# Performance work log

Measured on AMD Instinct MI355X. Metric: run time of the kernel, lower is better.

Reference implementation:

```python
import jax, jax.numpy as jnp
import numpy as np

DIM = 256
N_EMBED = 1024
COMMITMENT_COST = 0.25


def setup_inputs() -> dict:
    key = jax.random.key(0)
    k1, k2 = jax.random.split(key)
    z = jax.random.normal(k1, (16, 256, 64, 64), dtype=jnp.float32)
    # nn.Embedding weight initialized uniform(-1/n_embed, 1/n_embed)
    embed = jax.random.uniform(k2, (N_EMBED, DIM), dtype=jnp.float32,
                               minval=-1.0 / N_EMBED, maxval=1.0 / N_EMBED)
    return {"z": z, "embed": embed}


def reference(z, embed):
    sg = jax.lax.stop_gradient
    # NCHW -> NHWC, flatten spatial+batch to tokens
    zp = jnp.transpose(z, (0, 2, 3, 1))            # [B,H,W,C]
    zf = zp.reshape(-1, DIM)                        # [N, C]
    # squared euclidean distances via expansion: |z|^2 + |e|^2 - 2 z.e
    d = (jnp.sum(zf * zf, axis=1, keepdims=True)
         + jnp.sum(embed * embed, axis=1)
         - 2.0 * zf @ embed.T)                      # [N, K]
    idx = jnp.argmin(d, axis=1)                     # [N]
    min_encodings = jax.nn.one_hot(idx, N_EMBED, dtype=zf.dtype)  # [N, K]
    # direct gather == one-hot @ embed (same math, one HBM pass)
    z_q = embed[idx].reshape(zp.shape)              # [B,H,W,C]
    loss = (jnp.mean((sg(z_q) - zp) ** 2)
            + COMMITMENT_COST * jnp.mean((z_q - sg(zp)) ** 2))
    # straight-through estimator
    z_q_st = zp + sg(z_q - zp)
    e_mean = jnp.mean(min_encodings, axis=0)
    perplexity = jnp.exp(-jnp.sum(e_mean * jnp.log(e_mean + 1e-10)))
    z_q_out = jnp.transpose(z_q_st, (0, 3, 1, 2))   # back to NCHW
    return (loss, z_q_out, perplexity, min_encodings, idx[:, None])
```

## Files before the change

kernel.cpp:

```cpp
#include <hip/hip_runtime.h>
#include <math.h>

#define DIM    256
#define K_EMB  1024
#define HW     4096
#define CHW    1048576
#define N_TOK  65536
#define NELEM  16777216

#define OUT_LOSS 0
#define OUT_ZQ   1
#define OUT_PERP 16777217
#define OUT_MENC 16777218LL
#define OUT_IDX  83886082

#define TAU  1.5e-4f
#define WIN  6e-4f

typedef short short8  __attribute__((ext_vector_type(8)));
typedef float floatx4 __attribute__((ext_vector_type(4)));

#define A_OFF     2LL
#define EH_OFF    (A_OFF + 16777216LL)
#define FLAGS_OFF (EH_OFF + 131072LL)
#define SB_OFF    33554430LL

__device__ __forceinline__ unsigned short f2bf(float f) {
    unsigned int u = __float_as_uint(f);
    return (unsigned short)((u + 0x7FFFu + ((u >> 16) & 1u)) >> 16);
}
__device__ __forceinline__ float bf2f(unsigned short h) {
    return __uint_as_float(((unsigned int)h) << 16);
}

__device__ __forceinline__ float np_pair128(const float* p) {
    float r[8];
    #pragma unroll
    for (int j = 0; j < 8; ++j) r[j] = p[j];
    for (int i = 8; i < 128; i += 8)
        #pragma unroll
        for (int j = 0; j < 8; ++j) r[j] = __fadd_rn(r[j], p[i + j]);
    return __fadd_rn(__fadd_rn(__fadd_rn(r[0], r[1]), __fadd_rn(r[2], r[3])),
                     __fadd_rn(__fadd_rn(r[4], r[5]), __fadd_rn(r[6], r[7])));
}
__device__ __forceinline__ float np_pair256(const float* p) {
    return __fadd_rn(np_pair128(p), np_pair128(p + 128));
}

__global__ void t2_np_kernel(const float* __restrict__ embed, float* __restrict__ t2,
                             unsigned short* __restrict__ Eh) {
    int k = blockIdx.x * 256 + threadIdx.x;
    if (k >= K_EMB) return;
    const float* e = embed + (size_t)k * DIM;
    float p[256];
    for (int c = 0; c < DIM; c += 4) {
        float4 v = *(const float4*)(e + c);
        p[c]     = __fmul_rn(v.x, v.x);
        p[c + 1] = __fmul_rn(v.y, v.y);
        p[c + 2] = __fmul_rn(v.z, v.z);
        p[c + 3] = __fmul_rn(v.w, v.w);
    }
    t2[k] = np_pair256(p);
    unsigned short* dst = Eh + (size_t)k * DIM;
    for (int c0 = 0; c0 < DIM; c0 += 8) {
        short8 vh;
        #pragma unroll
        for (int u = 0; u < 8; ++u) vh[u] = (short)f2bf(e[c0 + u]);
        *(short8*)(dst + c0) = vh;
    }
}

__global__ void prep_z(const float* __restrict__ z, unsigned short* __restrict__ Ap) {
    const int tid = threadIdx.x;
    const int w   = tid & 63;
    const int j   = tid >> 6;
    const int n   = blockIdx.x * 64 + w;
    const int b   = n >> 12;
    const int rem = n & 4095;
    const float* zp = z + (size_t)b * CHW + rem;
    unsigned short* dst = Ap + (size_t)n * 512;
    for (int g = 0; g < 8; ++g) {
        int c0 = j * 64 + g * 8;
        short8 vh, vl;
        #pragma unroll
        for (int u = 0; u < 8; ++u) {
            float v = zp[(size_t)(c0 + u) * HW];
            unsigned short h = f2bf(v);
            vh[u] = (short)h;
            vl[u] = (short)f2bf(v - bf2f(h));
        }
        *(short8*)(dst + c0)       = vh;
        *(short8*)(dst + 256 + c0) = vl;
    }
}

__launch_bounds__(256, 4)
__global__ void vq_mfma(const unsigned short* __restrict__ Ap,
                        const unsigned short* __restrict__ Eh,
                        const float* __restrict__ t2g,
                        float* __restrict__ out,
                        unsigned int* __restrict__ nflag,
                        int* __restrict__ flags,
                        unsigned short* __restrict__ Sb) {
    __shared__ unsigned short lds_b[32 * 264];
    __shared__ float t2_lds[K_EMB];
    __shared__ unsigned short score_lds[64 * 40];

    const int tid  = threadIdx.x;
    const int lane = tid & 63;
    const int wv   = tid >> 6;
    const int l15  = lane & 15;
    const int quad = lane >> 4;
    const int m0   = blockIdx.x * 64;

    for (int i = tid; i < K_EMB; i += 256) t2_lds[i] = t2g[i];

    short8 a[16];
    const short8* arow = (const short8*)(Ap + (size_t)(m0 + wv * 16 + l15) * 512);
    #pragma unroll
    for (int kc = 0; kc < 16; ++kc) a[kc] = arow[kc * 4 + quad];

    float bs[4], ss[4]; int bk[4];
    float sc0[4], sc1[4];
    #pragma unroll
    for (int r = 0; r < 4; ++r) { bs[r] = 3.4e38f; ss[r] = 3.4e38f; bk[r] = 0; }

    const int srow = tid >> 3;
    const int scol = (tid & 7) * 32;
    const int tt = tid >> 2, ch = tid & 3;

    for (int it = 0; it < 32; ++it) {
        const int n0 = it * 32;
        __syncthreads();
        {
            const short8* g = (const short8*)(Eh + (size_t)(n0 + srow) * 256 + scol);
            short8* l = (short8*)(lds_b + srow * 264 + scol);
            short8 v0 = g[0], v1 = g[1], v2 = g[2], v3 = g[3];
            l[0] = v0; l[1] = v1; l[2] = v2; l[3] = v3;
        }
        if (it > 0) {
            #pragma unroll
            for (int r = 0; r < 4; ++r) {
                int row = wv * 16 + quad * 4 + r;
                score_lds[row * 40 + l15]      = f2bf(sc0[r]);
                score_lds[row * 40 + 16 + l15] = f2bf(sc1[r]);
            }
        }
        __syncthreads();
        if (it > 0) {
            short8 v = *(short8*)(score_lds + tt * 40 + ch * 8);
            *(short8*)(Sb + (size_t)(m0 + tt) * 1024 + (n0 - 32) + ch * 8) = v;
        }
        floatx4 acc0 = {0.f, 0.f, 0.f, 0.f};
        floatx4 acc1 = {0.f, 0.f, 0.f, 0.f};
        #pragma unroll
        for (int kc = 0; kc < 8; ++kc) {
            short8 b0 = *(const short8*)(lds_b + l15 * 264 + kc * 32 + quad * 8);
            short8 b1 = *(const short8*)(lds_b + (16 + l15) * 264 + kc * 32 + quad * 8);
            acc0 = __builtin_amdgcn_mfma_f32_16x16x32_bf16(a[kc],     b0, acc0, 0, 0, 0);
            acc1 = __builtin_amdgcn_mfma_f32_16x16x32_bf16(a[kc],     b1, acc1, 0, 0, 0);
            acc0 = __builtin_amdgcn_mfma_f32_16x16x32_bf16(a[8 + kc], b0, acc0, 0, 0, 0);
            acc1 = __builtin_amdgcn_mfma_f32_16x16x32_bf16(a[8 + kc], b1, acc1, 0, 0, 0);
        }
        float t20 = t2_lds[n0 + l15];
        float t21 = t2_lds[n0 + 16 + l15];
        #pragma unroll
        for (int r = 0; r < 4; ++r) {
            float s0 = fmaf(-2.0f, acc0[r], t20);
            sc0[r] = s0;
            if (s0 < bs[r]) { ss[r] = bs[r]; bs[r] = s0; bk[r] = n0 + l15; }
            else if (s0 < ss[r]) ss[r] = s0;
            float s1 = fmaf(-2.0f, acc1[r], t21);
            sc1[r] = s1;
            if (s1 < bs[r]) { ss[r] = bs[r]; bs[r] = s1; bk[r] = n0 + 16 + l15; }
            else if (s1 < ss[r]) ss[r] = s1;
        }
    }
    __syncthreads();
    #pragma unroll
    for (int r = 0; r < 4; ++r) {
        int row = wv * 16 + quad * 4 + r;
        score_lds[row * 40 + l15]      = f2bf(sc0[r]);
        score_lds[row * 40 + 16 + l15] = f2bf(sc1[r]);
    }
    __syncthreads();
    {
        short8 v = *(short8*)(score_lds + tt * 40 + ch * 8);
        *(short8*)(Sb + (size_t)(m0 + tt) * 1024 + 992 + ch * 8) = v;
    }

    #pragma unroll
    for (int r = 0; r < 4; ++r) {
        for (int mo = 1; mo < 16; mo <<= 1) {
            float obs = __shfl_xor(bs[r], mo, 64);
            float oss = __shfl_xor(ss[r], mo, 64);
            int   obk = __shfl_xor(bk[r], mo, 64);
            if (obs < bs[r] || (obs == bs[r] && obk < bk[r])) {
                ss[r] = fminf(bs[r], oss); bs[r] = obs; bk[r] = obk;
            } else {
                ss[r] = fminf(ss[r], obs);
            }
        }
        if (l15 == 0) {
            int ntok = m0 + wv * 16 + quad * 4 + r;
            out[OUT_IDX + ntok] = (float)bk[r];
            if (ss[r] - bs[r] < TAU) {
                unsigned int slot = atomicAdd(nflag, 1u);
                flags[slot] = ntok;
            }
        }
    }
}

__launch_bounds__(256)
__global__ void refine_v2(const float* __restrict__ z, const float* __restrict__ embed,
                          const float* __restrict__ t2g, float* __restrict__ out,
                          const unsigned int* __restrict__ nflag,
                          const int* __restrict__ flags,
                          const unsigned short* __restrict__ Sb) {
    __shared__ float pp4[4][256];
    __shared__ int   ccnt[4];
    __shared__ int   clist[4][32];

    const int lane = threadIdx.x & 63;
    const int wv   = threadIdx.x >> 6;
    const int wid  = blockIdx.x * 4 + wv;
    const int nf   = (int)*nflag;

    for (int i = wid; i < nf; i += gridDim.x * 4) {
        const int n   = flags[i];
        const int b   = n >> 12;
        const int rem = n & 4095;

        const unsigned short* srow = Sb + (size_t)n * 1024;
        short8 u0 = *(const short8*)(srow + lane * 16);
        short8 u1 = *(const short8*)(srow + lane * 16 + 8);
        float sv[16];
        #pragma unroll
        for (int j = 0; j < 8; ++j) { sv[j] = bf2f((unsigned short)u0[j]); sv[8 + j] = bf2f((unsigned short)u1[j]); }
        float lmin = sv[0];
        #pragma unroll
        for (int j = 1; j < 16; ++j) lmin = fminf(lmin, sv[j]);
        for (int mo = 1; mo < 64; mo <<= 1) lmin = fminf(lmin, __shfl_xor(lmin, mo, 64));
        const float thr = lmin + WIN;

        if (lane == 0) ccnt[wv] = 0;
        __asm__ volatile("s_waitcnt lgkmcnt(0)" ::: "memory");
        #pragma unroll
        for (int j = 0; j < 16; ++j) {
            if (sv[j] <= thr) {
                int pos = atomicAdd(&ccnt[wv], 1);
                if (pos < 32) clist[wv][pos] = lane * 16 + j;
            }
        }
        __asm__ volatile("s_waitcnt lgkmcnt(0)" ::: "memory");
        int cnt = ccnt[wv];
        if (cnt > 32) cnt = 32;

        const float* zt = z + (size_t)b * CHW + rem;
        double zd[4]; float zf[4];
        #pragma unroll
        for (int u = 0; u < 4; ++u) {
            float v = zt[(size_t)(lane + u * 64) * HW];
            zf[u] = v; zd[u] = (double)v;
            pp4[wv][lane + u * 64] = __fmul_rn(v, v);
        }
        __asm__ volatile("s_waitcnt lgkmcnt(0)" ::: "memory");
        float rj = 0.0f;
        if (lane < 16) {
            int jj = lane & 7, half = lane >> 3;
            const float* p = &pp4[wv][half * 128 + jj];
            rj = p[0];
            #pragma unroll
            for (int ii = 1; ii < 16; ++ii) rj = __fadd_rn(rj, p[ii * 8]);
        }
        float v0 = __shfl(rj, 0, 64), v1 = __shfl(rj, 1, 64), v2 = __shfl(rj, 2, 64), v3 = __shfl(rj, 3, 64);
        float v4 = __shfl(rj, 4, 64), v5 = __shfl(rj, 5, 64), v6 = __shfl(rj, 6, 64), v7 = __shfl(rj, 7, 64);
        float h0 = __fadd_rn(__fadd_rn(__fadd_rn(v0, v1), __fadd_rn(v2, v3)),
                             __fadd_rn(__fadd_rn(v4, v5), __fadd_rn(v6, v7)));
        v0 = __shfl(rj,  8, 64); v1 = __shfl(rj,  9, 64); v2 = __shfl(rj, 10, 64); v3 = __shfl(rj, 11, 64);
        v4 = __shfl(rj, 12, 64); v5 = __shfl(rj, 13, 64); v6 = __shfl(rj, 14, 64); v7 = __shfl(rj, 15, 64);
        float h1 = __fadd_rn(__fadd_rn(__fadd_rn(v0, v1), __fadd_rn(v2, v3)),
                             __fadd_rn(__fadd_rn(v4, v5), __fadd_rn(v6, v7)));
        const float t1 = __fadd_rn(h0, h1);

        float bd = 3.4e38f; int bkk = 1 << 30;
        for (int ci = 0; ci < cnt; ++ci) {
            int k = clist[wv][ci];
            const float* e = embed + (size_t)k * DIM;
            double s = 0.0;
            #pragma unroll
            for (int u = 0; u < 4; ++u) s = fma(zd[u], (double)e[lane + u * 64], s);
            for (int mo = 1; mo < 64; mo <<= 1) s += __shfl_xor(s, mo, 64);
            float rho = (float)s;
            float d = __fadd_rn(__fadd_rn(t1, t2g[k]), -__fmul_rn(2.0f, rho));
            if (d < bd || (d == bd && k < bkk)) { bd = d; bkk = k; }
        }
        if (lane == 0) out[OUT_IDX + n] = (float)bkk;
    }
}

__launch_bounds__(256)
__global__ void zq_loss_kernel(const float* __restrict__ z, const float* __restrict__ embed,
                               float* __restrict__ out, unsigned int* __restrict__ counts,
                               float* __restrict__ loss_sum) {
    const int tid = threadIdx.x;
    const int blk = blockIdx.x;
    const int b   = blk >> 7;
    const int h   = (blk >> 1) & 63;
    const int wh  = blk & 1;
    const int w   = tid & 31;
    const int cs  = tid >> 5;
    const int n   = blk * 32 + w;

    const int myk = (int)out[OUT_IDX + n];
    if (tid < 32) atomicAdd(&counts[myk], 1u);

    const float* erow = embed + (size_t)myk * DIM;
    const float* zt = z   + (size_t)b * CHW + h * 64 + wh * 32;
    float*       zq = out + OUT_ZQ + (size_t)b * CHW + h * 64 + wh * 32;
    float lsum = 0.0f;
    for (int c = cs; c < DIM; c += 8) {
        float v  = erow[c];
        float dz = v - zt[(size_t)c * HW + w];
        lsum = fmaf(dz, dz, lsum);
        zq[(size_t)c * HW + w] = v;
    }
    #pragma unroll
    for (int off = 32; off > 0; off >>= 1) lsum += __shfl_down(lsum, off, 64);
    if ((tid & 63) == 0) atomicAdd(loss_sum, lsum);
}

__global__ void min_enc_kernel(float* __restrict__ out) {
    long long gid = (long long)blockIdx.x * 256 + threadIdx.x;
    int n  = (int)(gid >> 9);
    int j2 = (int)(gid & 511);
    int k0 = j2 << 1;
    int id = (int)out[OUT_IDX + n];
    float2 v;
    v.x = (k0     == id) ? 1.0f : 0.0f;
    v.y = (k0 + 1 == id) ? 1.0f : 0.0f;
    *(float2*)(out + OUT_MENC + (long long)n * K_EMB + k0) = v;
}

__global__ void finalize_kernel(const unsigned int* __restrict__ counts,
                                const float* __restrict__ loss_sum,
                                float* __restrict__ out) {
    __shared__ float red[256];
    int tid = threadIdx.x;
    float hsum = 0.0f;
    for (int k = tid; k < K_EMB; k += 256) {
        float p = (float)counts[k] * (1.0f / 65536.0f);
        hsum += p * logf(p + 1e-10f);
    }
    red[tid] = hsum;
    __syncthreads();
    for (int s = 128; s > 0; s >>= 1) {
        if (tid < s) red[tid] += red[tid + s];
        __syncthreads();
    }
    if (tid == 0) {
        out[OUT_PERP] = expf(-red[0]);
        out[OUT_LOSS] = loss_sum[0] * 1.25f * (1.0f / (float)NELEM);
    }
}

extern "C" void kernel_launch(void* const* d_in, const int* in_sizes, int n_in,
                              void* d_out, int out_size, void* d_ws, size_t ws_size,
                              hipStream_t stream) {
    const float* z     = (const float*)d_in[0];
    const float* embed = (const float*)d_in[1];
    float* out = (float*)d_out;

    unsigned int* counts = (unsigned int*)d_ws;
    float* loss_sum      = (float*)((char*)d_ws + 4096);
    unsigned int* nflag  = (unsigned int*)((char*)d_ws + 4100);
    float* t2g           = (float*)((char*)d_ws + 8192);

    float* scr = out + OUT_MENC;
    unsigned short* Ap = (unsigned short*)(scr + A_OFF);
    unsigned short* Eh = (unsigned short*)(scr + EH_OFF);
    int*            fl = (int*)(scr + FLAGS_OFF);
    unsigned short* Sb = (unsigned short*)(scr + SB_OFF);

    hipMemsetAsync(d_ws, 0, 4104, stream);
    t2_np_kernel   <<<dim3(4),      dim3(256), 0, stream>>>(embed, t2g, Eh);
    prep_z         <<<dim3(1024),   dim3(256), 0, stream>>>(z, Ap);
    vq_mfma        <<<dim3(1024),   dim3(256), 0, stream>>>(Ap, Eh, t2g, out, nflag, fl, Sb);
    refine_v2      <<<dim3(512),    dim3(256), 0, stream>>>(z, embed, t2g, out, nflag, fl, Sb);
    zq_loss_kernel <<<dim3(2048),   dim3(256), 0, stream>>>(z, embed, out, counts, loss_sum);
    min_enc_kernel <<<dim3(131072), dim3(256), 0, stream>>>(out);
    finalize_kernel<<<dim3(1),      dim3(256), 0, stream>>>(counts, loss_sum, out);
}
```

Measured before the change: 785.7 us.

## Fuse z prep and one-hot writes into MFMA kernel; recompute refine candidates via MFMA

```diff
diff --git a/kernel.cpp b/kernel.cpp
--- a/kernel.cpp
+++ b/kernel.cpp
@@ -15,15 +15,15 @@
 #define OUT_IDX  83886082
 
 #define TAU  1.5e-4f
-#define WIN  6e-4f
+
+#define TAIL_ROW0  65216
+#define FLAGS_OFF  66781184LL
+#define FBS_OFF    66846720LL
+#define EH_OFF     66912258LL
 
 typedef short short8  __attribute__((ext_vector_type(8)));
 typedef float floatx4 __attribute__((ext_vector_type(4)));
-
-#define A_OFF     2LL
-#define EH_OFF    (A_OFF + 16777216LL)
-#define FLAGS_OFF (EH_OFF + 131072LL)
-#define SB_OFF    33554430LL
+typedef float floatx2 __attribute__((ext_vector_type(2)));
 
 __device__ __forceinline__ unsigned short f2bf(float f) {
     unsigned int u = __float_as_uint(f);
@@ -45,6 +45,22 @@
 }
 __device__ __forceinline__ float np_pair256(const float* p) {
     return __fadd_rn(np_pair128(p), np_pair128(p + 128));
+}
+
+__device__ __forceinline__ void build_frags(const float* __restrict__ zp, int quad, short8* a) {
+    #pragma unroll
+    for (int kc = 0; kc < 8; ++kc) {
+        short8 vh, vl;
+        #pragma unroll
+        for (int u = 0; u < 8; ++u) {
+            float v = __builtin_nontemporal_load(zp + (size_t)(kc * 32 + quad * 8 + u) * HW);
+            unsigned short h = f2bf(v);
+            vh[u] = (short)h;
+            vl[u] = (short)f2bf(v - bf2f(h));
+        }
+        a[kc]     = vh;
+        a[8 + kc] = vl;
+    }
 }
 
 __global__ void t2_np_kernel(const float* __restrict__ embed, float* __restrict__ t2,
@@ -70,41 +86,17 @@
     }
 }
 
-__global__ void prep_z(const float* __restrict__ z, unsigned short* __restrict__ Ap) {
-    const int tid = threadIdx.x;
-    const int w   = tid & 63;
-    const int j   = tid >> 6;
-    const int n   = blockIdx.x * 64 + w;
-    const int b   = n >> 12;
-    const int rem = n & 4095;
-    const float* zp = z + (size_t)b * CHW + rem;
-    unsigned short* dst = Ap + (size_t)n * 512;
-    for (int g = 0; g < 8; ++g) {
-        int c0 = j * 64 + g * 8;
-        short8 vh, vl;
-        #pragma unroll
-        for (int u = 0; u < 8; ++u) {
-            float v = zp[(size_t)(c0 + u) * HW];
-            unsigned short h = f2bf(v);
-            vh[u] = (short)h;
-            vl[u] = (short)f2bf(v - bf2f(h));
-        }
-        *(short8*)(dst + c0)       = vh;
-        *(short8*)(dst + 256 + c0) = vl;
-    }
-}
-
 __launch_bounds__(256, 4)
-__global__ void vq_mfma(const unsigned short* __restrict__ Ap,
+__global__ void vq_mfma(const float* __restrict__ z,
                         const unsigned short* __restrict__ Eh,
                         const float* __restrict__ t2g,
                         float* __restrict__ out,
                         unsigned int* __restrict__ nflag,
                         int* __restrict__ flags,
-                        unsigned short* __restrict__ Sb) {
+                        float* __restrict__ fbs) {
     __shared__ unsigned short lds_b[32 * 264];
     __shared__ float t2_lds[K_EMB];
-    __shared__ unsigned short score_lds[64 * 40];
+    __shared__ int midx[64];
 
     const int tid  = threadIdx.x;
     const int lane = tid & 63;
@@ -116,18 +108,17 @@
     for (int i = tid; i < K_EMB; i += 256) t2_lds[i] = t2g[i];
 
     short8 a[16];
-    const short8* arow = (const short8*)(Ap + (size_t)(m0 + wv * 16 + l15) * 512);
-    #pragma unroll
-    for (int kc = 0; kc < 16; ++kc) a[kc] = arow[kc * 4 + quad];
+    {
+        const int n = m0 + wv * 16 + l15;
+        build_frags(z + (size_t)(n >> 12) * CHW + (n & 4095), quad, a);
+    }
 
     float bs[4], ss[4]; int bk[4];
-    float sc0[4], sc1[4];
     #pragma unroll
     for (int r = 0; r < 4; ++r) { bs[r] = 3.4e38f; ss[r] = 3.4e38f; bk[r] = 0; }
 
     const int srow = tid >> 3;
     const int scol = (tid & 7) * 32;
-    const int tt = tid >> 2, ch = tid & 3;
 
     for (int it = 0; it < 32; ++it) {
         const int n0 = it * 32;
@@ -138,19 +129,7 @@
             short8 v0 = g[0], v1 = g[1], v2 = g[2], v3 = g[3];
             l[0] = v0; l[1] = v1; l[2] = v2; l[3] = v3;
         }
-        if (it > 0) {
-            #pragma unroll
-            for (int r = 0; r < 4; ++r) {
-                int row = wv * 16 + quad * 4 + r;
-                score_lds[row * 40 + l15]      = f2bf(sc0[r]);
-                score_lds[row * 40 + 16 + l15] = f2bf(sc1[r]);
-            }
-        }
-        __syncthreads();
-        if (it > 0) {
-            short8 v = *(short8*)(score_lds + tt * 40 + ch * 8);
-            *(short8*)(Sb + (size_t)(m0 + tt) * 1024 + (n0 - 32) + ch * 8) = v;
-        }
+        __syncthreads();
         floatx4 acc0 = {0.f, 0.f, 0.f, 0.f};
         floatx4 acc1 = {0.f, 0.f, 0.f, 0.f};
         #pragma unroll
@@ -167,26 +146,12 @@
         #pragma unroll
         for (int r = 0; r < 4; ++r) {
             float s0 = fmaf(-2.0f, acc0[r], t20);
-            sc0[r] = s0;
             if (s0 < bs[r]) { ss[r] = bs[r]; bs[r] = s0; bk[r] = n0 + l15; }
             else if (s0 < ss[r]) ss[r] = s0;
             float s1 = fmaf(-2.0f, acc1[r], t21);
-            sc1[r] = s1;
             if (s1 < bs[r]) { ss[r] = bs[r]; bs[r] = s1; bk[r] = n0 + 16 + l15; }
             else if (s1 < ss[r]) ss[r] = s1;
         }
-    }
-    __syncthreads();
-    #pragma unroll
-    for (int r = 0; r < 4; ++r) {
-        int row = wv * 16 + quad * 4 + r;
-        score_lds[row * 40 + l15]      = f2bf(sc0[r]);
-        score_lds[row * 40 + 16 + l15] = f2bf(sc1[r]);
-    }
-    __syncthreads();
-    {
-        short8 v = *(short8*)(score_lds + tt * 40 + ch * 8);
-        *(short8*)(Sb + (size_t)(m0 + tt) * 1024 + 992 + ch * 8) = v;
     }
 
     #pragma unroll
@@ -202,102 +167,188 @@
             }
         }
         if (l15 == 0) {
-            int ntok = m0 + wv * 16 + quad * 4 + r;
-            out[OUT_IDX + ntok] = (float)bk[r];
+            int tl = wv * 16 + quad * 4 + r;
+            out[OUT_IDX + m0 + tl] = (float)bk[r];
+            midx[tl] = bk[r];
             if (ss[r] - bs[r] < TAU) {
                 unsigned int slot = atomicAdd(nflag, 1u);
-                flags[slot] = ntok;
-            }
+                flags[slot] = m0 + tl;
+                fbs[slot]   = bs[r];
+            }
+        }
+    }
+
+    if (blockIdx.x < (TAIL_ROW0 / 64)) {
+        __syncthreads();
+        #pragma unroll 1
+        for (int j = 0; j < 64; ++j) {
+            const int id = midx[j];
+            floatx2* dst = (floatx2*)(out + OUT_MENC + (size_t)(m0 + j) * K_EMB);
+            int c0 = tid * 2;
+            floatx2 v;  v.x  = (c0 == id)       ? 1.0f : 0.0f;  v.y  = (c0 + 1 == id)  ? 1.0f : 0.0f;
+            __builtin_nontemporal_store(v, dst + tid);
+            int c1 = c0 + 512;
+            floatx2 w2; w2.x = (c1 == id)       ? 1.0f : 0.0f;  w2.y = (c1 + 1 == id)  ? 1.0f : 0.0f;
+            __builtin_nontemporal_store(w2, dst + 256 + tid);
         }
     }
 }
 
 __launch_bounds__(256)
-__global__ void refine_v2(const float* __restrict__ z, const float* __restrict__ embed,
-                          const float* __restrict__ t2g, float* __restrict__ out,
-                          const unsigned int* __restrict__ nflag,
-                          const int* __restrict__ flags,
-                          const unsigned short* __restrict__ Sb) {
+__global__ void refine_mfma(const float* __restrict__ z, const float* __restrict__ embed,
+                            const unsigned short* __restrict__ Eh,
+                            const float* __restrict__ t2g, float* __restrict__ out,
+                            const unsigned int* __restrict__ nflag,
+                            const int* __restrict__ flags,
+                            const float* __restrict__ fbs) {
+    __shared__ unsigned short lds_b[32 * 264];
+    __shared__ float t2_lds[K_EMB];
+    __shared__ int   ftok[64];
+    __shared__ float fbest[64];
+    __shared__ int   ccnt[64];
+    __shared__ int   clist[64][32];
     __shared__ float pp4[4][256];
-    __shared__ int   ccnt[4];
-    __shared__ int   clist[4][32];
-
-    const int lane = threadIdx.x & 63;
-    const int wv   = threadIdx.x >> 6;
-    const int wid  = blockIdx.x * 4 + wv;
+
+    const int tid  = threadIdx.x;
+    const int lane = tid & 63;
+    const int wv   = tid >> 6;
+    const int l15  = lane & 15;
+    const int quad = lane >> 4;
     const int nf   = (int)*nflag;
 
-    for (int i = wid; i < nf; i += gridDim.x * 4) {
-        const int n   = flags[i];
-        const int b   = n >> 12;
-        const int rem = n & 4095;
-
-        const unsigned short* srow = Sb + (size_t)n * 1024;
-        short8 u0 = *(const short8*)(srow + lane * 16);
-        short8 u1 = *(const short8*)(srow + lane * 16 + 8);
-        float sv[16];
-        #pragma unroll
-        for (int j = 0; j < 8; ++j) { sv[j] = bf2f((unsigned short)u0[j]); sv[8 + j] = bf2f((unsigned short)u1[j]); }
-        float lmin = sv[0];
-        #pragma unroll
-        for (int j = 1; j < 16; ++j) lmin = fminf(lmin, sv[j]);
-        for (int mo = 1; mo < 64; mo <<= 1) lmin = fminf(lmin, __shfl_xor(lmin, mo, 64));
-        const float thr = lmin + WIN;
-
-        if (lane == 0) ccnt[wv] = 0;
-        __asm__ volatile("s_waitcnt lgkmcnt(0)" ::: "memory");
-        #pragma unroll
-        for (int j = 0; j < 16; ++j) {
-            if (sv[j] <= thr) {
-                int pos = atomicAdd(&ccnt[wv], 1);
-                if (pos < 32) clist[wv][pos] = lane * 16 + j;
-            }
-        }
-        __asm__ volatile("s_waitcnt lgkmcnt(0)" ::: "memory");
-        int cnt = ccnt[wv];
-        if (cnt > 32) cnt = 32;
-
-        const float* zt = z + (size_t)b * CHW + rem;
-        double zd[4]; float zf[4];
-        #pragma unroll
-        for (int u = 0; u < 4; ++u) {
-            float v = zt[(size_t)(lane + u * 64) * HW];
-            zf[u] = v; zd[u] = (double)v;
-            pp4[wv][lane + u * 64] = __fmul_rn(v, v);
-        }
-        __asm__ volatile("s_waitcnt lgkmcnt(0)" ::: "memory");
-        float rj = 0.0f;
-        if (lane < 16) {
-            int jj = lane & 7, half = lane >> 3;
-            const float* p = &pp4[wv][half * 128 + jj];
-            rj = p[0];
+    for (int i = tid; i < K_EMB; i += 256) t2_lds[i] = t2g[i];
+
+    const int srow = tid >> 3;
+    const int scol = (tid & 7) * 32;
+
+    for (int base = blockIdx.x * 64; base < nf; base += gridDim.x * 64) {
+        __syncthreads();
+        if (tid < 64) {
+            int ii  = base + tid;
+            int src = (ii < nf) ? ii : base;
+            ftok[tid]  = flags[src];
+            fbest[tid] = fbs[src];
+            ccnt[tid]  = 0;
+        }
+        __syncthreads();
+
+        short8 a[16];
+        {
+            const int n = ftok[wv * 16 + l15];
+            build_frags(z + (size_t)(n >> 12) * CHW + (n & 4095), quad, a);
+        }
+        float ftb[4];
+        #pragma unroll
+        for (int r = 0; r < 4; ++r) ftb[r] = fbest[wv * 16 + quad * 4 + r] + TAU;
+
+        for (int it = 0; it < 32; ++it) {
+            const int n0 = it * 32;
+            __syncthreads();
+            {
+                const short8* g = (const short8*)(Eh + (size_t)(n0 + srow) * 256 + scol);
+                short8* l = (short8*)(lds_b + srow * 264 + scol);
+                short8 v0 = g[0], v1 = g[1], v2 = g[2], v3 = g[3];
+                l[0] = v0; l[1] = v1; l[2] = v2; l[3] = v3;
+            }
+            __syncthreads();
+            floatx4 acc0 = {0.f, 0.f, 0.f, 0.f};
+            floatx4 acc1 = {0.f, 0.f, 0.f, 0.f};
             #pragma unroll
-            for (int ii = 1; ii < 16; ++ii) rj = __fadd_rn(rj, p[ii * 8]);
-        }
-        float v0 = __shfl(rj, 0, 64), v1 = __shfl(rj, 1, 64), v2 = __shfl(rj, 2, 64), v3 = __shfl(rj, 3, 64);
-        float v4 = __shfl(rj, 4, 64), v5 = __shfl(rj, 5, 64), v6 = __shfl(rj, 6, 64), v7 = __shfl(rj, 7, 64);
-        float h0 = __fadd_rn(__fadd_rn(__fadd_rn(v0, v1), __fadd_rn(v2, v3)),
-                             __fadd_rn(__fadd_rn(v4, v5), __fadd_rn(v6, v7)));
-        v0 = __shfl(rj,  8, 64); v1 = __shfl(rj,  9, 64); v2 = __shfl(rj, 10, 64); v3 = __shfl(rj, 11, 64);
-        v4 = __shfl(rj, 12, 64); v5 = __shfl(rj, 13, 64); v6 = __shfl(rj, 14, 64); v7 = __shfl(rj, 15, 64);
-        float h1 = __fadd_rn(__fadd_rn(__fadd_rn(v0, v1), __fadd_rn(v2, v3)),
-                             __fadd_rn(__fadd_rn(v4, v5), __fadd_rn(v6, v7)));
-        const float t1 = __fadd_rn(h0, h1);
-
-        float bd = 3.4e38f; int bkk = 1 << 30;
-        for (int ci = 0; ci < cnt; ++ci) {
-            int k = clist[wv][ci];
-            const float* e = embed + (size_t)k * DIM;
-            double s = 0.0;
+            for (int kc = 0; kc < 8; ++kc) {
+                short8 b0 = *(const short8*)(lds_b + l15 * 264 + kc * 32 + quad * 8);
+                short8 b1 = *(const short8*)(lds_b + (16 + l15) * 264 + kc * 32 + quad * 8);
+                acc0 = __builtin_amdgcn_mfma_f32_16x16x32_bf16(a[kc],     b0, acc0, 0, 0, 0);
+                acc1 = __builtin_amdgcn_mfma_f32_16x16x32_bf16(a[kc],     b1, acc1, 0, 0, 0);
+                acc0 = __builtin_amdgcn_mfma_f32_16x16x32_bf16(a[8 + kc], b0, acc0, 0, 0, 0);
+                acc1 = __builtin_amdgcn_mfma_f32_16x16x32_bf16(a[8 + kc], b1, acc1, 0, 0, 0);
+            }
+            float t20 = t2_lds[n0 + l15];
+            float t21 = t2_lds[n0 + 16 + l15];
             #pragma unroll
-            for (int u = 0; u < 4; ++u) s = fma(zd[u], (double)e[lane + u * 64], s);
-            for (int mo = 1; mo < 64; mo <<= 1) s += __shfl_xor(s, mo, 64);
-            float rho = (float)s;
-            float d = __fadd_rn(__fadd_rn(t1, t2g[k]), -__fmul_rn(2.0f, rho));
-            if (d < bd || (d == bd && k < bkk)) { bd = d; bkk = k; }
-        }
-        if (lane == 0) out[OUT_IDX + n] = (float)bkk;
-    }
+            for (int r = 0; r < 4; ++r) {
+                const int trow = wv * 16 + quad * 4 + r;
+                float s0 = fmaf(-2.0f, acc0[r], t20);
+                if (s0 <= ftb[r]) {
+                    int pos = atomicAdd(&ccnt[trow], 1);
+                    if (pos < 32) clist[trow][pos] = n0 + l15;
+                }
+                float s1 = fmaf(-2.0f, acc1[r], t21);
+                if (s1 <= ftb[r]) {
+                    int pos = atomicAdd(&ccnt[trow], 1);
+                    if (pos < 32) clist[trow][pos] = n0 + 16 + l15;
+                }
+            }
+        }
+        __syncthreads();
+
+        for (int j = wv * 16; j < wv * 16 + 16; ++j) {
+            if (base + j >= nf) break;
+            const int n = ftok[j];
+            int cnt = ccnt[j]; if (cnt > 32) cnt = 32;
+
+            const float* zt = z + (size_t)(n >> 12) * CHW + (n & 4095);
+            double zd[4];
+            #pragma unroll
+            for (int u = 0; u < 4; ++u) {
+                float v = zt[(size_t)(lane + u * 64) * HW];
+                zd[u] = (double)v;
+                pp4[wv][lane + u * 64] = __fmul_rn(v, v);
+            }
+            __asm__ volatile("s_waitcnt lgkmcnt(0)" ::: "memory");
+            float rj = 0.0f;
+            if (lane < 16) {
+                int jj = lane & 7, half = lane >> 3;
+                const float* p = &pp4[wv][half * 128 + jj];
+                rj = p[0];
+                #pragma unroll
+                for (int ii = 1; ii < 16; ++ii) rj = __fadd_rn(rj, p[ii * 8]);
+            }
+            float v0 = __shfl(rj, 0, 64), v1 = __shfl(rj, 1, 64), v2 = __shfl(rj, 2, 64), v3 = __shfl(rj, 3, 64);
+            float v4 = __shfl(rj, 4, 64), v5 = __shfl(rj, 5, 64), v6 = __shfl(rj, 6, 64), v7 = __shfl(rj, 7, 64);
+            float h0 = __fadd_rn(__fadd_rn(__fadd_rn(v0, v1), __fadd_rn(v2, v3)),
+                                 __fadd_rn(__fadd_rn(v4, v5), __fadd_rn(v6, v7)));
+            v0 = __shfl(rj,  8, 64); v1 = __shfl(rj,  9, 64); v2 = __shfl(rj, 10, 64); v3 = __shfl(rj, 11, 64);
+            v4 = __shfl(rj, 12, 64); v5 = __shfl(rj, 13, 64); v6 = __shfl(rj, 14, 64); v7 = __shfl(rj, 15, 64);
+            float h1 = __fadd_rn(__fadd_rn(__fadd_rn(v0, v1), __fadd_rn(v2, v3)),
+                                 __fadd_rn(__fadd_rn(v4, v5), __fadd_rn(v6, v7)));
+            const float t1 = __fadd_rn(h0, h1);
+
+            float bd = 3.4e38f; int bkk = 1 << 30;
+            for (int ci = 0; ci < cnt; ++ci) {
+                int k = clist[j][ci];
+                const float* e = embed + (size_t)k * DIM;
+                double s = 0.0;
+                #pragma unroll
+                for (int u = 0; u < 4; ++u) s = fma(zd[u], (double)e[lane + u * 64], s);
+                for (int mo = 1; mo < 64; mo <<= 1) s += __shfl_xor(s, mo, 64);
+                float rho = (float)s;
+                float d = __fadd_rn(__fadd_rn(t1, t2_lds[k]), -__fmul_rn(2.0f, rho));
+                if (d < bd || (d == bd && k < bkk)) { bd = d; bkk = k; }
+            }
+            if (lane == 0) {
+                int old = (int)out[OUT_IDX + n];
+                if (bkk != old) {
+                    out[OUT_IDX + n] = (float)bkk;
+                    if (n < TAIL_ROW0) {
+                        out[OUT_MENC + (size_t)n * K_EMB + old] = 0.0f;
+                        out[OUT_MENC + (size_t)n * K_EMB + bkk] = 1.0f;
+                    }
+                }
+            }
+        }
+    }
+}
+
+__global__ void menc_tail(float* __restrict__ out) {
+    const int row = TAIL_ROW0 + blockIdx.x;
+    const int id  = (int)out[OUT_IDX + row];
+    floatx2* dst = (floatx2*)(out + OUT_MENC + (size_t)row * K_EMB);
+    int c0 = threadIdx.x * 2;
+    floatx2 v;  v.x  = (c0 == id)      ? 1.0f : 0.0f;  v.y  = (c0 + 1 == id) ? 1.0f : 0.0f;
+    dst[threadIdx.x] = v;
+    int c1 = c0 + 512;
+    floatx2 w;  w.x  = (c1 == id)      ? 1.0f : 0.0f;  w.y  = (c1 + 1 == id) ? 1.0f : 0.0f;
+    dst[256 + threadIdx.x] = w;
 }
 
 __launch_bounds__(256)
@@ -331,18 +382,6 @@
     if ((tid & 63) == 0) atomicAdd(loss_sum, lsum);
 }
 
-__global__ void min_enc_kernel(float* __restrict__ out) {
-    long long gid = (long long)blockIdx.x * 256 + threadIdx.x;
-    int n  = (int)(gid >> 9);
-    int j2 = (int)(gid & 511);
-    int k0 = j2 << 1;
-    int id = (int)out[OUT_IDX + n];
-    float2 v;
-    v.x = (k0     == id) ? 1.0f : 0.0f;
-    v.y = (k0 + 1 == id) ? 1.0f : 0.0f;
-    *(float2*)(out + OUT_MENC + (long long)n * K_EMB + k0) = v;
-}
-
 __global__ void finalize_kernel(const unsigned int* __restrict__ counts,
                                 const float* __restrict__ loss_sum,
                                 float* __restrict__ out) {
@@ -378,17 +417,15 @@
     float* t2g           = (float*)((char*)d_ws + 8192);
 
     float* scr = out + OUT_MENC;
-    unsigned short* Ap = (unsigned short*)(scr + A_OFF);
+    int*            fl = (int*)(scr + FLAGS_OFF);
+    float*          fb = (float*)(scr + FBS_OFF);
     unsigned short* Eh = (unsigned short*)(scr + EH_OFF);
-    int*            fl = (int*)(scr + FLAGS_OFF);
-    unsigned short* Sb = (unsigned short*)(scr + SB_OFF);
-
-    hipMemsetAsync(d_ws, 0, 4104, stream);
-    t2_np_kernel   <<<dim3(4),      dim3(256), 0, stream>>>(embed, t2g, Eh);
-    prep_z         <<<dim3(1024),   dim3(256), 0, stream>>>(z, Ap);
-    vq_mfma        <<<dim3(1024),   dim3(256), 0, stream>>>(Ap, Eh, t2g, out, nflag, fl, Sb);
-    refine_v2      <<<dim3(512),    dim3(256), 0, stream>>>(z, embed, t2g, out, nflag, fl, Sb);
-    zq_loss_kernel <<<dim3(2048),   dim3(256), 0, stream>>>(z, embed, out, counts, loss_sum);
-    min_enc_kernel <<<dim3(131072), dim3(256), 0, stream>>>(out);
-    finalize_kernel<<<dim3(1),      dim3(256), 0, stream>>>(counts, loss_sum, out);
-}
+
+    (void)hipMemsetAsync(d_ws, 0, 4104, stream);
+    t2_np_kernel   <<<dim3(4),    dim3(256), 0, stream>>>(embed, t2g, Eh);
+    vq_mfma        <<<dim3(1024), dim3(256), 0, stream>>>(z, Eh, t2g, out, nflag, fl, fb);
+    refine_mfma    <<<dim3(128),  dim3(256), 0, stream>>>(z, embed, Eh, t2g, out, nflag, fl, fb);
+    menc_tail      <<<dim3(320),  dim3(256), 0, stream>>>(out);
+    zq_loss_kernel <<<dim3(2048), dim3(256), 0, stream>>>(z, embed, out, counts, loss_sum);
+    finalize_kernel<<<dim3(1),    dim3(256), 0, stream>>>(counts, loss_sum, out);
+}
```

New measurement: 775.8 us. Within noise of the previous version (-1.3%).
